# Performance work log

Hardware: AMD Instinct MI355X
Metric: run time of the kernel (lower is better)

Reference implementation:

```python
import jax, jax.numpy as jnp
import numpy as np

B = 512; H = 84; W = 84; K = 20; DEPTH = 24; EMB = 512
FCS = 7 * 7 * 64
FLOW_C = 0.01


def _init(key, shape, fan_in):
    return jax.random.normal(key, shape, jnp.float32) * (1.0 / np.sqrt(fan_in))


def setup_inputs() -> dict:
    key = jax.random.key(0)
    ks = jax.random.split(key, 22)
    return {
        "inp": jax.random.normal(ks[0], (B, 2, H, W), jnp.float32),
        "cw1": _init(ks[1], (32, 2, 8, 8), 2 * 8 * 8),
        "cb1": jnp.zeros((32,), jnp.float32),
        "cw2": _init(ks[2], (64, 32, 4, 4), 32 * 4 * 4),
        "cb2": jnp.zeros((64,), jnp.float32),
        "cw3": _init(ks[3], (64, 64, 3, 3), 64 * 3 * 3),
        "cb3": jnp.zeros((64,), jnp.float32),
        "fcw": _init(ks[4], (EMB, FCS), FCS),
        "fcb": jnp.zeros((EMB,), jnp.float32),
        "otw": _init(ks[5], (K * 2, EMB), EMB),
        "otb": jnp.zeros((K * 2,), jnp.float32),
        "ctw": _init(ks[6], (2, EMB), EMB),
        "ctb": jnp.zeros((2,), jnp.float32),
        "m1w": _init(ks[7], (21 * 21 * DEPTH, EMB), EMB),
        "m1b": jnp.zeros((21 * 21 * DEPTH,), jnp.float32),
        "c1w": _init(ks[8], (DEPTH, DEPTH, 3, 3), DEPTH * 9),
        "c1b": jnp.zeros((DEPTH,), jnp.float32),
        "c2w": _init(ks[9], (DEPTH, DEPTH, 3, 3), DEPTH * 9),
        "c2b": jnp.zeros((DEPTH,), jnp.float32),
        "c3w": _init(ks[10], (K, DEPTH, 1, 1), DEPTH),
        "c3b": jnp.zeros((K,), jnp.float32),
    }


def _conv(x, w, b, stride, pad):
    y = jax.lax.conv_general_dilated(
        x, w, (stride, stride), [(pad, pad), (pad, pad)],
        dimension_numbers=("NCHW", "OIHW", "NCHW"))
    return y + b[None, :, None, None]


def _up_mat(in_s, out_s):
    # bilinear, align_corners=True (torch UpsamplingBilinear2d)
    pos = jnp.arange(out_s, dtype=jnp.float32) * ((in_s - 1) / (out_s - 1))
    lo = jnp.clip(jnp.floor(pos).astype(jnp.int32), 0, in_s - 2)
    w = pos - lo.astype(jnp.float32)
    r = jnp.arange(out_s)
    M = jnp.zeros((out_s, in_s), jnp.float32)
    M = M.at[r, lo].add(1.0 - w).at[r, lo + 1].add(w)
    return M


def reference(inp, cw1, cb1, cw2, cb2, cw3, cb3, fcw, fcb, otw, otb,
              ctw, ctb, m1w, m1b, c1w, c1b, c2w, c2b, c3w, c3b):
    bs = inp.shape[0]
    # CNN encoder
    h1 = jax.nn.relu(_conv(inp, cw1, cb1, 4, 0))
    h2 = jax.nn.relu(_conv(h1, cw2, cb2, 2, 0))
    h3 = jax.nn.relu(_conv(h2, cw3, cb3, 1, 0))
    feat = h3.reshape(bs, -1)                              # [B, 3136]
    x = jax.nn.relu(feat @ fcw.T + fcb)                    # [B, EMB]
    # mask decoder
    m = (x @ m1w.T + m1b).reshape(bs, DEPTH, 21, 21)
    M42 = _up_mat(21, 42)
    m = jnp.einsum('bchw,Hh,Ww->bcHW', m, M42, M42)        # 21->42
    m = jax.nn.relu(m + _conv(m, c1w, c1b, 1, 1))
    M84 = _up_mat(42, 84)
    m = jnp.einsum('bchw,Hh,Ww->bcHW', m, M84, M84)        # 42->84
    m = jax.nn.relu(m + _conv(m, c2w, c2b, 1, 1))
    m = jax.nn.sigmoid(_conv(m, c3w, c3b, 1, 0))           # [B, K, 84, 84]
    # per-object translations -> flow
    ot = (x @ otw.T + otb).reshape(bs, K, 2)
    flow = jnp.einsum('bkhw,bkt->bthw', m, ot).reshape(bs, 2, H * W)
    ct = (x @ ctw.T + ctb)[:, :, None]                     # [B,2,1]
    flat_flow = flow + ct
    img_size_f = FLOW_C * jnp.array([[float(H)], [float(W)]], jnp.float32)
    # mesh grid: row 0 = y (row index), row 1 = x (col index)
    gy = jnp.repeat(jnp.arange(H, dtype=jnp.float32), W)
    gx = jnp.tile(jnp.arange(W, dtype=jnp.float32), H)
    grid = jnp.stack([gy, gx], 0)                          # [2, H*W]
    coords = img_size_f * flat_flow + grid
    ys = coords[:, 0, :].reshape(-1)                       # [B*H*W]
    xs = coords[:, 1, :].reshape(-1)
    # manual bilinear gather from second input frame
    src = inp[:, 1, :, :].reshape(-1)                      # [B*H*W] flat image
    x0 = jnp.clip(jnp.floor(xs).astype(jnp.int32), 0, W - 1)
    x1 = jnp.clip(x0 + 1, 0, W - 1)
    y0 = jnp.clip(jnp.floor(ys).astype(jnp.int32), 0, H - 1)
    y1 = jnp.clip(y0 + 1, 0, H - 1)
    base = jnp.repeat(jnp.arange(bs, dtype=jnp.int32) * (H * W), H * W)
    Ia = src[base + y0 * W + x0]
    Ib = src[base + y1 * W + x0]
    Ic = src[base + y0 * W + x1]
    Id = src[base + y1 * W + x1]
    xc = jnp.clip(xs, 0.0, float(W - 1))
    yc = jnp.clip(ys, 0.0, float(H - 1))
    x0f = x0.astype(jnp.float32); x1f = x1.astype(jnp.float32)
    y0f = y0.astype(jnp.float32); y1f = y1.astype(jnp.float32)
    out = ((x1f - xc) * (y1f - yc) * Ia + (x1f - xc) * (yc - y0f) * Ib +
           (xc - x0f) * (y1f - yc) * Ic + (xc - x0f) * (yc - y0f) * Id)
    return out.reshape(bs, 1, H, W)
```

## Files before the change

kernel.cpp:

```cpp
#include <hip/hip_runtime.h>
#include <math.h>

namespace {

typedef float f32x2 __attribute__((ext_vector_type(2)));
typedef float f32x4 __attribute__((ext_vector_type(4)));

#if defined(__has_builtin)
#if __has_builtin(__builtin_elementwise_fma)
#define HAVE_EW_FMA 1
#endif
#endif

__device__ __forceinline__ f32x2 pkfma(f32x2 a, f32x2 b, f32x2 c) {
#ifdef HAVE_EW_FMA
  return __builtin_elementwise_fma(a, b, c);
#else
  return a * b + c;
#endif
}
__device__ __forceinline__ f32x4 fma4(f32x4 a, f32x4 b, f32x4 c) {
#ifdef HAVE_EW_FMA
  return __builtin_elementwise_fma(a, b, c);
#else
  return a * b + c;
#endif
}

constexpr int IMS  = 84;
constexpr int NPIX = IMS * IMS;
constexpr int KOBJ = 20;

constexpr size_t OFF_X    = 0;
constexpr size_t OFF_OT   = 262144;
constexpr size_t OFF_CT   = 282624;
constexpr size_t OFF_WT2  = 283648;
constexpr size_t OFF_WT3  = 316416;
constexpr size_t OFF_M0   = 353280;
constexpr size_t OFF_R1   = 5772288;
constexpr size_t OFF_H1   = OFF_R1;
constexpr size_t OFF_H2   = 12325888;
constexpr size_t OFF_FEAT = 14980096;
constexpr size_t OFF_M1WT = OFF_H1;
constexpr size_t OFF_M1BT = OFF_H1 + 5419008;

__global__ void transpose_w(const float* __restrict__ w, float* __restrict__ wt,
                            int OC, int CKK) {
  int idx = blockIdx.x * 256 + threadIdx.x;
  if (idx < OC * CKK) {
    int oc = idx / CKK, ckk = idx % CKK;
    wt[ckk * OC + oc] = w[idx];
  }
}

__global__ __launch_bounds__(128) void permute_m1(
    const float* __restrict__ m1w, const float* __restrict__ m1b,
    float* __restrict__ wT, float* __restrict__ bT) {
  const int n = blockIdx.x;
  const int c = n / 441, rem = n % 441;
  const int np = rem * 24 + c;
  const float4* src = (const float4*)(m1w + (size_t)n * 512);
  float4* dst = (float4*)(wT + (size_t)np * 512);
  dst[threadIdx.x] = src[threadIdx.x];
  if (threadIdx.x == 0) bT[np] = m1b[n];
}

__global__ __launch_bounds__(256) void conv1_k(
    const float* __restrict__ inp, const float* __restrict__ w,
    const float* __restrict__ bias, float* __restrict__ out) {
  __shared__ __align__(16) float sIn[NPIX];
  __shared__ __align__(16) float sW[128 * 32];
  const int b = blockIdx.x, t = threadIdx.x;
  for (int i = t; i < 4096; i += 256) {
    int oc = i >> 7, ckk = i & 127;
    sW[ckk * 32 + oc] = w[i];
  }
  const float* ip = inp + (size_t)b * 2 * NPIX;
  const int oc0 = (t & 7) * 4;
  const int pg  = t >> 3;
  int ibase[13];
#pragma unroll
  for (int k = 0; k < 13; k++) {
    int p = pg + 32 * k; if (p > 399) p = 399;
    ibase[k] = (p / 20) * 4 * 84 + (p % 20) * 4;
  }
  f32x2 acc[13][2];
#pragma unroll
  for (int k = 0; k < 13; k++) { acc[k][0] = f32x2{0.f, 0.f}; acc[k][1] = f32x2{0.f, 0.f}; }
  for (int c = 0; c < 2; c++) {
    __syncthreads();
    for (int i = t; i < NPIX; i += 256) sIn[i] = ip[c * NPIX + i];
    __syncthreads();
    for (int u = 0; u < 8; u++) {
#pragma unroll
      for (int v = 0; v < 8; v++) {
        const float4 wv = *(const float4*)&sW[((c * 8 + u) * 8 + v) * 32 + oc0];
        const f32x2 w0 = {wv.x, wv.y}, w1 = {wv.z, wv.w};
        const int off = u * 84 + v;
#pragma unroll
        for (int k = 0; k < 13; k++) {
          float x = sIn[off + ibase[k]];
          f32x2 xv = {x, x};
          acc[k][0] = pkfma(w0, xv, acc[k][0]);
          acc[k][1] = pkfma(w1, xv, acc[k][1]);
        }
      }
    }
  }
  float b0 = bias[oc0], b1 = bias[oc0+1], b2 = bias[oc0+2], b3 = bias[oc0+3];
  float* op = out + (size_t)b * 32 * 400;
#pragma unroll
  for (int k = 0; k < 13; k++) {
    int p = pg + 32 * k;
    if (p < 400) {
      op[(oc0+0)*400 + p] = fmaxf(acc[k][0][0] + b0, 0.f);
      op[(oc0+1)*400 + p] = fmaxf(acc[k][0][1] + b1, 0.f);
      op[(oc0+2)*400 + p] = fmaxf(acc[k][1][0] + b2, 0.f);
      op[(oc0+3)*400 + p] = fmaxf(acc[k][1][1] + b3, 0.f);
    }
  }
}

__global__ __launch_bounds__(256) void conv2_k(
    const float* __restrict__ in, const float* __restrict__ wt,
    const float* __restrict__ bias, float* __restrict__ out) {
  __shared__ float sIn[32 * 400];
  const int b = blockIdx.x, t = threadIdx.x;
  const float* ip = in + (size_t)b * 12800;
  for (int i = t; i < 12800; i += 256) sIn[i] = ip[i];
  __syncthreads();
  const int oc0 = (t & 7) * 8;
  const int pg  = t >> 3;
  int base[3];
#pragma unroll
  for (int k = 0; k < 3; k++) {
    int p = pg + 32 * k; if (p > 80) p = 80;
    base[k] = (p / 9) * 40 + (p % 9) * 2;
  }
  f32x2 acc[3][4];
#pragma unroll
  for (int k = 0; k < 3; k++)
#pragma unroll
    for (int o = 0; o < 4; o++) acc[k][o] = f32x2{0.f, 0.f};
  for (int c = 0; c < 32; c++) {
#pragma unroll
    for (int u = 0; u < 4; u++)
#pragma unroll
      for (int v = 0; v < 4; v++) {
        const float* wp = wt + ((c * 4 + u) * 4 + v) * 64 + oc0;
        float4 wa = *(const float4*)wp;
        float4 wb = *(const float4*)(wp + 4);
        const f32x2 w0 = {wa.x, wa.y}, w1 = {wa.z, wa.w};
        const f32x2 w2 = {wb.x, wb.y}, w3 = {wb.z, wb.w};
        int off = c * 400 + u * 20 + v;
#pragma unroll
        for (int k = 0; k < 3; k++) {
          float x = sIn[off + base[k]];
          f32x2 xv = {x, x};
          acc[k][0] = pkfma(w0, xv, acc[k][0]);
          acc[k][1] = pkfma(w1, xv, acc[k][1]);
          acc[k][2] = pkfma(w2, xv, acc[k][2]);
          acc[k][3] = pkfma(w3, xv, acc[k][3]);
        }
      }
  }
  float* op = out + (size_t)b * 5184;
#pragma unroll
  for (int k = 0; k < 3; k++) {
    int p = pg + 32 * k;
    if (p < 81) {
#pragma unroll
      for (int o = 0; o < 8; o++)
        op[(oc0+o)*81 + p] = fmaxf(acc[k][o >> 1][o & 1] + bias[oc0+o], 0.f);
    }
  }
}

__global__ __launch_bounds__(256) void conv3_k(
    const float* __restrict__ in, const float* __restrict__ wt,
    const float* __restrict__ bias, float* __restrict__ out) {
  __shared__ float sIn[64 * 81];
  const int b = blockIdx.x, t = threadIdx.x;
  const float* ip = in + (size_t)b * 5184;
  for (int i = t; i < 5184; i += 256) sIn[i] = ip[i];
  __syncthreads();
  const int oc0 = (t & 7) * 8;
  const int pg  = t >> 3;
  int base[2];
#pragma unroll
  for (int k = 0; k < 2; k++) {
    int p = pg + 32 * k; if (p > 48) p = 48;
    base[k] = (p / 7) * 9 + (p % 7);
  }
  f32x2 acc[2][4];
#pragma unroll
  for (int k = 0; k < 2; k++)
#pragma unroll
    for (int o = 0; o < 4; o++) acc[k][o] = f32x2{0.f, 0.f};
  for (int c = 0; c < 64; c++) {
#pragma unroll
    for (int u = 0; u < 3; u++)
#pragma unroll
      for (int v = 0; v < 3; v++) {
        const float* wp = wt + ((c * 3 + u) * 3 + v) * 64 + oc0;
        float4 wa = *(const float4*)wp;
        float4 wb = *(const float4*)(wp + 4);
        const f32x2 w0 = {wa.x, wa.y}, w1 = {wa.z, wa.w};
        const f32x2 w2 = {wb.x, wb.y}, w3 = {wb.z, wb.w};
        int off = c * 81 + u * 9 + v;
#pragma unroll
        for (int k = 0; k < 2; k++) {
          float x = sIn[off + base[k]];
          f32x2 xv = {x, x};
          acc[k][0] = pkfma(w0, xv, acc[k][0]);
          acc[k][1] = pkfma(w1, xv, acc[k][1]);
          acc[k][2] = pkfma(w2, xv, acc[k][2]);
          acc[k][3] = pkfma(w3, xv, acc[k][3]);
        }
      }
  }
  float* op = out + (size_t)b * 3136;
#pragma unroll
  for (int k = 0; k < 2; k++) {
    int p = pg + 32 * k;
    if (p < 49) {
#pragma unroll
      for (int o = 0; o < 8; o++)
        op[(oc0+o)*49 + p] = fmaxf(acc[k][o >> 1][o & 1] + bias[oc0+o], 0.f);
    }
  }
}

template<bool RELU>
__global__ __launch_bounds__(256) void gemm_k(
    const float* __restrict__ A, const float* __restrict__ Wm,
    const float* __restrict__ bias, float* __restrict__ C,
    int N, int K) {
  __shared__ __align__(16) float As[16][68];
  __shared__ __align__(16) float Ws[16][68];
  const int t = threadIdx.x;
  const int m0 = blockIdx.y * 64, n0 = blockIdx.x * 64;
  const int r  = t >> 2;
  const int kq = (t & 3) * 4;
  const int r0 = (t >> 4) * 4, c0 = (t & 15) * 4;
  f32x2 acc[4][2];
#pragma unroll
  for (int i = 0; i < 4; i++) { acc[i][0] = f32x2{0.f, 0.f}; acc[i][1] = f32x2{0.f, 0.f}; }
  for (int k0 = 0; k0 < K; k0 += 16) {
    float4 a = *(const float4*)(A + (size_t)(m0 + r) * K + k0 + kq);
    int wrow = n0 + r;
    float4 wv = make_float4(0.f, 0.f, 0.f, 0.f);
    if (wrow < N) wv = *(const float4*)(Wm + (size_t)wrow * K + k0 + kq);
    __syncthreads();
    As[kq+0][r] = a.x; As[kq+1][r] = a.y; As[kq+2][r] = a.z; As[kq+3][r] = a.w;
    Ws[kq+0][r] = wv.x; Ws[kq+1][r] = wv.y; Ws[kq+2][r] = wv.z; Ws[kq+3][r] = wv.w;
    __syncthreads();
#pragma unroll
    for (int kk = 0; kk < 16; kk++) {
      float4 av = *(const float4*)&As[kk][r0];
      float4 bv = *(const float4*)&Ws[kk][c0];
      const f32x2 b0 = {bv.x, bv.y}, b1 = {bv.z, bv.w};
      float ar[4] = {av.x, av.y, av.z, av.w};
#pragma unroll
      for (int i = 0; i < 4; i++) {
        f32x2 ai = {ar[i], ar[i]};
        acc[i][0] = pkfma(b0, ai, acc[i][0]);
        acc[i][1] = pkfma(b1, ai, acc[i][1]);
      }
    }
  }
#pragma unroll
  for (int i = 0; i < 4; i++) {
    int row = m0 + r0 + i;
#pragma unroll
    for (int j = 0; j < 4; j++) {
      int col = n0 + c0 + j;
      if (col < N) {
        float v = acc[i][j >> 1][j & 1] + bias[col];
        C[(size_t)row * N + col] = RELU ? fmaxf(v, 0.f) : v;
      }
    }
  }
}

__global__ __launch_bounds__(256) void gemm_splitk_k(
    const float* __restrict__ A, const float* __restrict__ Wm,
    float* __restrict__ Cpart, int N, int K, int Kslice) {
  __shared__ __align__(16) float As[16][68];
  __shared__ __align__(16) float Ws[16][68];
  const int t = threadIdx.x;
  const int m0 = blockIdx.y * 64, n0 = blockIdx.x * 64;
  const int kbeg = blockIdx.z * Kslice;
  const int kend = kbeg + Kslice;
  const int r  = t >> 2;
  const int kq = (t & 3) * 4;
  const int r0 = (t >> 4) * 4, c0 = (t & 15) * 4;
  f32x2 acc[4][2];
#pragma unroll
  for (int i = 0; i < 4; i++) { acc[i][0] = f32x2{0.f, 0.f}; acc[i][1] = f32x2{0.f, 0.f}; }
  for (int k0 = kbeg; k0 < kend; k0 += 16) {
    float4 a = *(const float4*)(A + (size_t)(m0 + r) * K + k0 + kq);
    float4 wv = *(const float4*)(Wm + (size_t)(n0 + r) * K + k0 + kq);
    __syncthreads();
    As[kq+0][r] = a.x; As[kq+1][r] = a.y; As[kq+2][r] = a.z; As[kq+3][r] = a.w;
    Ws[kq+0][r] = wv.x; Ws[kq+1][r] = wv.y; Ws[kq+2][r] = wv.z; Ws[kq+3][r] = wv.w;
    __syncthreads();
#pragma unroll
    for (int kk = 0; kk < 16; kk++) {
      float4 av = *(const float4*)&As[kk][r0];
      float4 bv = *(const float4*)&Ws[kk][c0];
      const f32x2 b0 = {bv.x, bv.y}, b1 = {bv.z, bv.w};
      float ar[4] = {av.x, av.y, av.z, av.w};
#pragma unroll
      for (int i = 0; i < 4; i++) {
        f32x2 ai = {ar[i], ar[i]};
        acc[i][0] = pkfma(b0, ai, acc[i][0]);
        acc[i][1] = pkfma(b1, ai, acc[i][1]);
      }
    }
  }
  float* cp = Cpart + (size_t)blockIdx.z * 512 * 512;
#pragma unroll
  for (int i = 0; i < 4; i++) {
    int row = m0 + r0 + i;
#pragma unroll
    for (int j = 0; j < 4; j++)
      cp[(size_t)row * N + n0 + c0 + j] = acc[i][j >> 1][j & 1];
  }
}

__global__ __launch_bounds__(256) void splitk_reduce_k(
    const float* __restrict__ Cpart, const float* __restrict__ bias,
    float* __restrict__ X) {
  int i4 = blockIdx.x * 256 + threadIdx.x;
  if (i4 < 65536) {
    int col4 = (i4 & 127) * 4;
    float4 p0 = *(const float4*)&Cpart[(size_t)i4 * 4];
    float4 p1 = *(const float4*)&Cpart[262144 + (size_t)i4 * 4];
    float4 p2 = *(const float4*)&Cpart[524288 + (size_t)i4 * 4];
    float4 p3 = *(const float4*)&Cpart[786432 + (size_t)i4 * 4];
    float4 bb = *(const float4*)&bias[col4];
    float4 o;
    o.x = fmaxf(p0.x + p1.x + p2.x + p3.x + bb.x, 0.f);
    o.y = fmaxf(p0.y + p1.y + p2.y + p3.y + bb.y, 0.f);
    o.z = fmaxf(p0.z + p1.z + p2.z + p3.z + bb.z, 0.f);
    o.w = fmaxf(p0.w + p1.w + p2.w + p3.w + bb.w, 0.f);
    *(float4*)&X[(size_t)i4 * 4] = o;
  }
}

__global__ __launch_bounds__(256) void gemm128_k(
    const float* __restrict__ A, const float* __restrict__ Wm,
    const float* __restrict__ bias, float* __restrict__ C,
    int N, int K) {
  __shared__ __align__(16) float As[16][132];
  __shared__ __align__(16) float Ws[16][132];
  const int t = threadIdx.x;
  const int m0 = blockIdx.y * 128, n0 = blockIdx.x * 128;
  const int lr = t >> 1;
  const int kq = (t & 1) * 8;
  const int r0 = (t >> 4) * 8, c0 = (t & 15) * 8;
  f32x2 acc[8][4];
#pragma unroll
  for (int i = 0; i < 8; i++)
#pragma unroll
    for (int j = 0; j < 4; j++) acc[i][j] = f32x2{0.f, 0.f};
  for (int k0 = 0; k0 < K; k0 += 16) {
    const float* ap = A + (size_t)(m0 + lr) * K + k0 + kq;
    float4 a0 = *(const float4*)ap;
    float4 a1 = *(const float4*)(ap + 4);
    int wrow = n0 + lr;
    float4 w0 = make_float4(0.f,0.f,0.f,0.f), w1 = make_float4(0.f,0.f,0.f,0.f);
    if (wrow < N) {
      const float* wp = Wm + (size_t)wrow * K + k0 + kq;
      w0 = *(const float4*)wp;
      w1 = *(const float4*)(wp + 4);
    }
    __syncthreads();
    As[kq+0][lr] = a0.x; As[kq+1][lr] = a0.y; As[kq+2][lr] = a0.z; As[kq+3][lr] = a0.w;
    As[kq+4][lr] = a1.x; As[kq+5][lr] = a1.y; As[kq+6][lr] = a1.z; As[kq+7][lr] = a1.w;
    Ws[kq+0][lr] = w0.x; Ws[kq+1][lr] = w0.y; Ws[kq+2][lr] = w0.z; Ws[kq+3][lr] = w0.w;
    Ws[kq+4][lr] = w1.x; Ws[kq+5][lr] = w1.y; Ws[kq+6][lr] = w1.z; Ws[kq+7][lr] = w1.w;
    __syncthreads();
#pragma unroll
    for (int kk = 0; kk < 16; kk++) {
      float4 av0 = *(const float4*)&As[kk][r0];
      float4 av1 = *(const float4*)&As[kk][r0 + 4];
      float4 bv0 = *(const float4*)&Ws[kk][c0];
      float4 bv1 = *(const float4*)&Ws[kk][c0 + 4];
      float ar[8] = {av0.x, av0.y, av0.z, av0.w, av1.x, av1.y, av1.z, av1.w};
      f32x2 br[4] = {{bv0.x, bv0.y}, {bv0.z, bv0.w}, {bv1.x, bv1.y}, {bv1.z, bv1.w}};
#pragma unroll
      for (int i = 0; i < 8; i++) {
        f32x2 ai = {ar[i], ar[i]};
#pragma unroll
        for (int j = 0; j < 4; j++) acc[i][j] = pkfma(br[j], ai, acc[i][j]);
      }
    }
  }
#pragma unroll
  for (int i = 0; i < 8; i++) {
    int row = m0 + r0 + i;
#pragma unroll
    for (int j = 0; j < 8; j++) {
      int col = n0 + c0 + j;
      if (col < N)
        C[(size_t)row * N + col] = acc[i][j >> 1][j & 1] + bias[col];
    }
  }
}

__global__ __launch_bounds__(384, 6) void upconv1_k(
    const float* __restrict__ X, const float* __restrict__ wt,
    const float* __restrict__ bias, float* __restrict__ outT) {
  constexpr int S_IN = 21, S_OUT = 42, TR = 6, UH = 8, UW = 44, NTILE = 7;
  __shared__ __align__(16) float sU[24 * UH * UW];
  const int b = blockIdx.x / NTILE;
  const int y0 = (blockIdx.x % NTILE) * TR;
  const int t = threadIdx.x;
  const float* xb = X + (size_t)b * 24 * S_IN * S_IN;
  const float sc = (float)(S_IN - 1) / (float)(S_OUT - 1);
  for (int rr = t; rr < UH * UW; rr += 384) {
    const int ry = rr / UW, cx = rr % UW;
    const int y = y0 + ry - 1, x = cx - 1;
    float* sdst = &sU[rr];
    if (y >= 0 && y < S_OUT && x >= 0 && x < S_OUT) {
      float py = y * sc, px = x * sc;
      int ly = (int)py; if (ly > S_IN - 2) ly = S_IN - 2;
      int lx = (int)px; if (lx > S_IN - 2) lx = S_IN - 2;
      float wy = py - (float)ly, wx = px - (float)lx;
      const f32x4 wx4 = {wx, wx, wx, wx};
      const f32x4 wy4 = {wy, wy, wy, wy};
      const float* p00 = xb + ((size_t)ly * S_IN + lx) * 24;
#pragma unroll
      for (int g = 0; g < 6; g++) {
        f32x4 q00 = *(const f32x4*)(p00 + 4 * g);
        f32x4 q01 = *(const f32x4*)(p00 + 24 + 4 * g);
        f32x4 q10 = *(const f32x4*)(p00 + 24 * S_IN + 4 * g);
        f32x4 q11 = *(const f32x4*)(p00 + 24 * S_IN + 24 + 4 * g);
        f32x4 ht = fma4(wx4, q01 - q00, q00);
        f32x4 hb = fma4(wx4, q11 - q10, q10);
        f32x4 v  = fma4(wy4, hb - ht, ht);
        sdst[(4*g + 0) * UH * UW] = v[0];
        sdst[(4*g + 1) * UH * UW] = v[1];
        sdst[(4*g + 2) * UH * UW] = v[2];
        sdst[(4*g + 3) * UH * UW] = v[3];
      }
    } else {
#pragma unroll
      for (int c = 0; c < 24; c++) sdst[c * UH * UW] = 0.f;
    }
  }
  __syncthreads();
  if (t < 252) {
    const int ry = t / 42, lx = t % 42;
    f32x2 acc[12];
#pragma unroll
    for (int j = 0; j < 12; j++) acc[j] = f32x2{0.f, 0.f};
    for (int ic = 0; ic < 24; ic++) {
      const float* urow = &sU[(ic * UH + ry) * UW + lx];
      const float* wp = wt + ic * 216;
#pragma unroll
      for (int ky = 0; ky < 3; ky++) {
        float x0v = urow[ky * UW + 0];
        float x1v = urow[ky * UW + 1];
        float x2v = urow[ky * UW + 2];
        f32x2 X0 = {x0v, x0v}, X1 = {x1v, x1v}, X2 = {x2v, x2v};
        const f32x2* wk2 = (const f32x2*)(wp + ky * 72);
#pragma unroll
        for (int j = 0; j < 12; j++)
          acc[j] = pkfma(wk2[j], X0,
                   pkfma(wk2[12 + j], X1,
                   pkfma(wk2[24 + j], X2, acc[j])));
      }
    }
    const int yy = y0 + ry;
    float* orow = outT + ((size_t)b * 1764 + yy * 42 + lx) * 24;
#pragma unroll
    for (int g = 0; g < 6; g++) {
      f32x4 u = { sU[((4*g + 0) * UH + ry + 1) * UW + lx + 1],
                  sU[((4*g + 1) * UH + ry + 1) * UW + lx + 1],
                  sU[((4*g + 2) * UH + ry + 1) * UW + lx + 1],
                  sU[((4*g + 3) * UH + ry + 1) * UW + lx + 1] };
      f32x4 a = {acc[2*g][0], acc[2*g][1], acc[2*g+1][0], acc[2*g+1][1]};
      f32x4 bb = *(const f32x4*)&bias[4*g];
      f32x4 s = u + a + bb;
      s[0] = fmaxf(s[0], 0.f); s[1] = fmaxf(s[1], 0.f);
      s[2] = fmaxf(s[2], 0.f); s[3] = fmaxf(s[3], 0.f);
      *(f32x4*)(orow + 4*g) = s;
    }
  }
}

__global__ __launch_bounds__(384, 6) void upconv2_final_k(
    const float* __restrict__ R1T, const float* __restrict__ inp,
    const float* __restrict__ wt, const float* __restrict__ bias,
    const float* __restrict__ c3w, const float* __restrict__ c3b,
    const float* __restrict__ ot, const float* __restrict__ ct,
    float* __restrict__ out) {
  constexpr int S_IN = 42, S_OUT = 84, TR = 6, UH = 8, TW = 42, UW = 44;
  __shared__ __align__(16) float sU[24 * UH * UW];
  const int blk = blockIdx.x;
  const int b = blk / 28;
  const int rr0 = blk % 28;
  const int y0 = (rr0 >> 1) * TR;
  const int x0 = (rr0 & 1) * TW;
  const int t = threadIdx.x;
  const float* xb = R1T + (size_t)b * 1764 * 24;
  const float sc = (float)(S_IN - 1) / (float)(S_OUT - 1);
  for (int rr = t; rr < UH * UW; rr += 384) {
    const int ry = rr / UW, cx = rr % UW;
    const int y = y0 + ry - 1, x = x0 + cx - 1;
    float* sdst = &sU[rr];
    if (y >= 0 && y < S_OUT && x >= 0 && x < S_OUT) {
      float py = y * sc, px = x * sc;
      int ly = (int)py; if (ly > S_IN - 2) ly = S_IN - 2;
      int lx = (int)px; if (lx > S_IN - 2) lx = S_IN - 2;
      float wy = py - (float)ly, wx = px - (float)lx;
      const f32x4 wx4 = {wx, wx, wx, wx};
      const f32x4 wy4 = {wy, wy, wy, wy};
      const float* p00 = xb + ((size_t)ly * S_IN + lx) * 24;
#pragma unroll
      for (int g = 0; g < 6; g++) {
        f32x4 q00 = *(const f32x4*)(p00 + 4 * g);
        f32x4 q01 = *(const f32x4*)(p00 + 24 + 4 * g);
        f32x4 q10 = *(const f32x4*)(p00 + 24 * S_IN + 4 * g);
        f32x4 q11 = *(const f32x4*)(p00 + 24 * S_IN + 24 + 4 * g);
        f32x4 ht = fma4(wx4, q01 - q00, q00);
        f32x4 hb = fma4(wx4, q11 - q10, q10);
        f32x4 v  = fma4(wy4, hb - ht, ht);
        sdst[(4*g + 0) * UH * UW] = v[0];
        sdst[(4*g + 1) * UH * UW] = v[1];
        sdst[(4*g + 2) * UH * UW] = v[2];
        sdst[(4*g + 3) * UH * UW] = v[3];
      }
    } else {
#pragma unroll
      for (int c = 0; c < 24; c++) sdst[c * UH * UW] = 0.f;
    }
  }
  __syncthreads();
  if (t < 252) {
    const int ry = t / 42, lx = t % 42;
    f32x2 acc[12];
#pragma unroll
    for (int j = 0; j < 12; j++) acc[j] = f32x2{0.f, 0.f};
    for (int ic = 0; ic < 24; ic++) {
      const float* urow = &sU[(ic * UH + ry) * UW + lx];
      const float* wp = wt + ic * 216;
#pragma unroll
      for (int ky = 0; ky < 3; ky++) {
        float x0v = urow[ky * UW + 0];
        float x1v = urow[ky * UW + 1];
        float x2v = urow[ky * UW + 2];
        f32x2 X0 = {x0v, x0v}, X1 = {x1v, x1v}, X2 = {x2v, x2v};
        const f32x2* wk2 = (const f32x2*)(wp + ky * 72);
#pragma unroll
        for (int j = 0; j < 12; j++)
          acc[j] = pkfma(wk2[j], X0,
                   pkfma(wk2[12 + j], X1,
                   pkfma(wk2[24 + j], X2, acc[j])));
      }
    }
    f32x2 r[12];
#pragma unroll
    for (int j = 0; j < 12; j++) {
      f32x2 u2 = { sU[((2*j)   * UH + ry + 1) * UW + lx + 1],
                   sU[((2*j+1) * UH + ry + 1) * UW + lx + 1] };
      f32x2 b2 = *(const f32x2*)&bias[2*j];
      f32x2 s = u2 + acc[j] + b2;
      r[j][0] = fmaxf(s[0], 0.f);
      r[j][1] = fmaxf(s[1], 0.f);
    }
    f32x2 f2 = *(const f32x2*)&ct[b * 2];
    const f32x2* ot2 = (const f32x2*)(ot + b * 2 * KOBJ);
    for (int k = 0; k < KOBJ; k++) {
      f32x2 zv = {c3b[k], 0.f};
      const f32x2* cw2 = (const f32x2*)(c3w + k * 24);
#pragma unroll
      for (int j = 0; j < 12; j++) zv = pkfma(r[j], cw2[j], zv);
      float z = zv[0] + zv[1];
      float m = 1.f / (1.f + __expf(-z));
      f32x2 mv = {m, m};
      f2 = pkfma(mv, ot2[k], f2);
    }
    const int gy = y0 + ry, gx = x0 + lx;
    const float imgf = 0.01f * 84.0f;
    float ys = imgf * f2[0] + (float)gy;
    float xs = imgf * f2[1] + (float)gx;
    int ix0 = (int)floorf(xs); ix0 = ix0 < 0 ? 0 : (ix0 > 83 ? 83 : ix0);
    int iy0 = (int)floorf(ys); iy0 = iy0 < 0 ? 0 : (iy0 > 83 ? 83 : iy0);
    int ix1 = ix0 + 1 > 83 ? 83 : ix0 + 1;
    int iy1 = iy0 + 1 > 83 ? 83 : iy0 + 1;
    float xc = fminf(fmaxf(xs, 0.f), 83.f);
    float yc = fminf(fmaxf(ys, 0.f), 83.f);
    float wx1 = (float)ix1 - xc, wx0 = xc - (float)ix0;
    float wy1 = (float)iy1 - yc, wy0 = yc - (float)iy0;
    const float* src = inp + ((size_t)b * 2 + 1) * NPIX;
    float Ia = src[iy0 * 84 + ix0], Ib = src[iy1 * 84 + ix0];
    float Ic = src[iy0 * 84 + ix1], Id = src[iy1 * 84 + ix1];
    out[(size_t)b * NPIX + gy * 84 + gx] =
        wx1 * wy1 * Ia + wx1 * wy0 * Ib + wx0 * wy1 * Ic + wx0 * wy0 * Id;
  }
}

}

extern "C" void kernel_launch(void* const* d_in, const int* in_sizes, int n_in,
                              void* d_out, int out_size, void* d_ws, size_t ws_size,
                              hipStream_t stream) {
  const float* inp = (const float*)d_in[0];
  const float* cw1 = (const float*)d_in[1];
  const float* cb1 = (const float*)d_in[2];
  const float* cw2 = (const float*)d_in[3];
  const float* cb2 = (const float*)d_in[4];
  const float* cw3 = (const float*)d_in[5];
  const float* cb3 = (const float*)d_in[6];
  const float* fcw = (const float*)d_in[7];
  const float* fcb = (const float*)d_in[8];
  const float* otw = (const float*)d_in[9];
  const float* otb = (const float*)d_in[10];
  const float* ctw = (const float*)d_in[11];
  const float* ctb = (const float*)d_in[12];
  const float* m1w = (const float*)d_in[13];
  const float* m1b = (const float*)d_in[14];
  const float* c1w = (const float*)d_in[15];
  const float* c1b = (const float*)d_in[16];
  const float* c2w = (const float*)d_in[17];
  const float* c2b = (const float*)d_in[18];
  const float* c3w = (const float*)d_in[19];
  const float* c3b = (const float*)d_in[20];
  float* W = (float*)d_ws;
  float* out = (float*)d_out;

  transpose_w<<<(64 * 512 + 255) / 256, 256, 0, stream>>>(cw2, W + OFF_WT2, 64, 512);
  transpose_w<<<(64 * 576 + 255) / 256, 256, 0, stream>>>(cw3, W + OFF_WT3, 64, 576);
  conv1_k<<<512, 256, 0, stream>>>(inp, cw1, cb1, W + OFF_H1);
  conv2_k<<<512, 256, 0, stream>>>(W + OFF_H1, W + OFF_WT2, cb2, W + OFF_H2);
  permute_m1<<<10584, 128, 0, stream>>>(m1w, m1b, W + OFF_M1WT, W + OFF_M1BT);
  conv3_k<<<512, 256, 0, stream>>>(W + OFF_H2, W + OFF_WT3, cb3, W + OFF_FEAT);
  transpose_w<<<(24 * 216 + 255) / 256, 256, 0, stream>>>(c1w, W + OFF_WT2, 24, 216);
  transpose_w<<<(24 * 216 + 255) / 256, 256, 0, stream>>>(c2w, W + OFF_WT3, 24, 216);
  gemm_splitk_k<<<dim3(8, 8, 4), 256, 0, stream>>>(W + OFF_FEAT, fcw, W + OFF_M0,
                                                   512, 3136, 784);
  splitk_reduce_k<<<256, 256, 0, stream>>>(W + OFF_M0, fcb, W + OFF_X);
  gemm_k<false><<<dim3(1, 8), 256, 0, stream>>>(W + OFF_X, otw, otb, W + OFF_OT, 40, 512);
  gemm_k<false><<<dim3(1, 8), 256, 0, stream>>>(W + OFF_X, ctw, ctb, W + OFF_CT, 2, 512);
  gemm128_k<<<dim3(83, 4), 256, 0, stream>>>(W + OFF_X, W + OFF_M1WT, W + OFF_M1BT,
                                             W + OFF_M0, 10584, 512);
  upconv1_k<<<512 * 7, 384, 0, stream>>>(W + OFF_M0, W + OFF_WT2, c1b, W + OFF_R1);
  upconv2_final_k<<<512 * 28, 384, 0, stream>>>(W + OFF_R1, inp, W + OFF_WT3, c2b,
                                                c3w, c3b, W + OFF_OT, W + OFF_CT, out);
}
```

Before: 1.076 ms.

## Split conv output channels across thread pairs, each computing two rows

Both upconv kernels change their thread-to-work mapping. Each thread now computes half of the 24 output channels (split by thread parity) for two vertically adjacent output rows instead of all channels for one row. Each loaded input value feeds both rows and each weight load is shared across two pixels, which cuts shared-memory and weight reads per FMA. In the final kernel the 1x1 conv reduction is completed with a lane shuffle between the pair, and only one thread of the pair does the warp sampling. This changes register pressure and the weight-load pattern, and the warp phase leaves half the threads idle.

```diff
diff --git a/kernel.cpp b/kernel.cpp
--- a/kernel.cpp
+++ b/kernel.cpp
@@ -453,41 +453,71 @@
   }
   __syncthreads();
   if (t < 252) {
-    const int ry = t / 42, lx = t % 42;
-    f32x2 acc[12];
-#pragma unroll
-    for (int j = 0; j < 12; j++) acc[j] = f32x2{0.f, 0.f};
+    const int h = t & 1;
+    const int u = t >> 1;
+    const int lx = u % 42, q = u / 42;
+    const int pr0 = 2 * q, pr1 = pr0 + 1;
+    f32x2 a0[6], a1[6];
+#pragma unroll
+    for (int j = 0; j < 6; j++) { a0[j] = f32x2{0.f, 0.f}; a1[j] = f32x2{0.f, 0.f}; }
+    const float* wph = wt + h * 12;
     for (int ic = 0; ic < 24; ic++) {
-      const float* urow = &sU[(ic * UH + ry) * UW + lx];
-      const float* wp = wt + ic * 216;
-#pragma unroll
-      for (int ky = 0; ky < 3; ky++) {
-        float x0v = urow[ky * UW + 0];
-        float x1v = urow[ky * UW + 1];
-        float x2v = urow[ky * UW + 2];
-        f32x2 X0 = {x0v, x0v}, X1 = {x1v, x1v}, X2 = {x2v, x2v};
-        const f32x2* wk2 = (const f32x2*)(wp + ky * 72);
-#pragma unroll
-        for (int j = 0; j < 12; j++)
-          acc[j] = pkfma(wk2[j], X0,
-                   pkfma(wk2[12 + j], X1,
-                   pkfma(wk2[24 + j], X2, acc[j])));
-      }
-    }
-    const int yy = y0 + ry;
-    float* orow = outT + ((size_t)b * 1764 + yy * 42 + lx) * 24;
-#pragma unroll
-    for (int g = 0; g < 6; g++) {
-      f32x4 u = { sU[((4*g + 0) * UH + ry + 1) * UW + lx + 1],
-                  sU[((4*g + 1) * UH + ry + 1) * UW + lx + 1],
-                  sU[((4*g + 2) * UH + ry + 1) * UW + lx + 1],
-                  sU[((4*g + 3) * UH + ry + 1) * UW + lx + 1] };
-      f32x4 a = {acc[2*g][0], acc[2*g][1], acc[2*g+1][0], acc[2*g+1][1]};
-      f32x4 bb = *(const f32x4*)&bias[4*g];
-      f32x4 s = u + a + bb;
-      s[0] = fmaxf(s[0], 0.f); s[1] = fmaxf(s[1], 0.f);
-      s[2] = fmaxf(s[2], 0.f); s[3] = fmaxf(s[3], 0.f);
-      *(f32x4*)(orow + 4*g) = s;
+      const float* ub = &sU[(ic * UH + pr0) * UW + lx];
+      float v[4][3];
+#pragma unroll
+      for (int r = 0; r < 4; r++)
+#pragma unroll
+        for (int kx = 0; kx < 3; kx++)
+          v[r][kx] = ub[r * UW + kx];
+      const float* wpc = wph + ic * 216;
+#pragma unroll
+      for (int ky = 0; ky < 3; ky++)
+#pragma unroll
+        for (int kx = 0; kx < 3; kx++) {
+          const float* wp = wpc + (ky * 3 + kx) * 24;
+          const f32x4 wA = *(const f32x4*)wp;
+          const f32x4 wB = *(const f32x4*)(wp + 4);
+          const f32x4 wC = *(const f32x4*)(wp + 8);
+          const f32x2 w0 = {wA[0], wA[1]}, w1 = {wA[2], wA[3]};
+          const f32x2 w2 = {wB[0], wB[1]}, w3 = {wB[2], wB[3]};
+          const f32x2 w4 = {wC[0], wC[1]}, w5 = {wC[2], wC[3]};
+          const f32x2 X0 = {v[ky][kx], v[ky][kx]};
+          const f32x2 X1 = {v[ky + 1][kx], v[ky + 1][kx]};
+          a0[0] = pkfma(w0, X0, a0[0]); a1[0] = pkfma(w0, X1, a1[0]);
+          a0[1] = pkfma(w1, X0, a0[1]); a1[1] = pkfma(w1, X1, a1[1]);
+          a0[2] = pkfma(w2, X0, a0[2]); a1[2] = pkfma(w2, X1, a1[2]);
+          a0[3] = pkfma(w3, X0, a0[3]); a1[3] = pkfma(w3, X1, a1[3]);
+          a0[4] = pkfma(w4, X0, a0[4]); a1[4] = pkfma(w4, X1, a1[4]);
+          a0[5] = pkfma(w5, X0, a0[5]); a1[5] = pkfma(w5, X1, a1[5]);
+        }
+    }
+    const int cb = h * 12;
+    const f32x4 bb0 = *(const f32x4*)&bias[cb];
+    const f32x4 bb1 = *(const f32x4*)&bias[cb + 4];
+    const f32x4 bb2 = *(const f32x4*)&bias[cb + 8];
+#pragma unroll
+    for (int px = 0; px < 2; px++) {
+      const int pr = px ? pr1 : pr0;
+      const f32x2* aa = px ? a1 : a0;
+      float o[12];
+#pragma unroll
+      for (int j = 0; j < 6; j++) {
+        float c0v = sU[((cb + 2*j)     * UH + pr + 1) * UW + lx + 1];
+        float c1v = sU[((cb + 2*j + 1) * UH + pr + 1) * UW + lx + 1];
+        o[2*j]   = c0v + aa[j][0];
+        o[2*j+1] = c1v + aa[j][1];
+      }
+      float* orow = outT + ((size_t)b * 1764 + (y0 + pr) * 42 + lx) * 24 + cb;
+      f32x4 s0 = {o[0], o[1], o[2], o[3]};   s0 += bb0;
+      f32x4 s1 = {o[4], o[5], o[6], o[7]};   s1 += bb1;
+      f32x4 s2 = {o[8], o[9], o[10], o[11]}; s2 += bb2;
+#pragma unroll
+      for (int e = 0; e < 4; e++) {
+        s0[e] = fmaxf(s0[e], 0.f); s1[e] = fmaxf(s1[e], 0.f); s2[e] = fmaxf(s2[e], 0.f);
+      }
+      *(f32x4*)(orow)     = s0;
+      *(f32x4*)(orow + 4) = s1;
+      *(f32x4*)(orow + 8) = s2;
     }
   }
 }
@@ -541,66 +571,110 @@
   }
   __syncthreads();
   if (t < 252) {
-    const int ry = t / 42, lx = t % 42;
-    f32x2 acc[12];
-#pragma unroll
-    for (int j = 0; j < 12; j++) acc[j] = f32x2{0.f, 0.f};
+    const int h = t & 1;
+    const int u = t >> 1;
+    const int lx = u % 42, q = u / 42;
+    const int pr0 = 2 * q, pr1 = pr0 + 1;
+    f32x2 a0[6], a1[6];
+#pragma unroll
+    for (int j = 0; j < 6; j++) { a0[j] = f32x2{0.f, 0.f}; a1[j] = f32x2{0.f, 0.f}; }
+    const float* wph = wt + h * 12;
     for (int ic = 0; ic < 24; ic++) {
-      const float* urow = &sU[(ic * UH + ry) * UW + lx];
-      const float* wp = wt + ic * 216;
-#pragma unroll
-      for (int ky = 0; ky < 3; ky++) {
-        float x0v = urow[ky * UW + 0];
-        float x1v = urow[ky * UW + 1];
-        float x2v = urow[ky * UW + 2];
-        f32x2 X0 = {x0v, x0v}, X1 = {x1v, x1v}, X2 = {x2v, x2v};
-        const f32x2* wk2 = (const f32x2*)(wp + ky * 72);
-#pragma unroll
-        for (int j = 0; j < 12; j++)
-          acc[j] = pkfma(wk2[j], X0,
-                   pkfma(wk2[12 + j], X1,
-                   pkfma(wk2[24 + j], X2, acc[j])));
-      }
-    }
-    f32x2 r[12];
-#pragma unroll
-    for (int j = 0; j < 12; j++) {
-      f32x2 u2 = { sU[((2*j)   * UH + ry + 1) * UW + lx + 1],
-                   sU[((2*j+1) * UH + ry + 1) * UW + lx + 1] };
-      f32x2 b2 = *(const f32x2*)&bias[2*j];
-      f32x2 s = u2 + acc[j] + b2;
-      r[j][0] = fmaxf(s[0], 0.f);
-      r[j][1] = fmaxf(s[1], 0.f);
-    }
-    f32x2 f2 = *(const f32x2*)&ct[b * 2];
-    const f32x2* ot2 = (const f32x2*)(ot + b * 2 * KOBJ);
+      const float* ub = &sU[(ic * UH + pr0) * UW + lx];
+      float v[4][3];
+#pragma unroll
+      for (int r = 0; r < 4; r++)
+#pragma unroll
+        for (int kx = 0; kx < 3; kx++)
+          v[r][kx] = ub[r * UW + kx];
+      const float* wpc = wph + ic * 216;
+#pragma unroll
+      for (int ky = 0; ky < 3; ky++)
+#pragma unroll
+        for (int kx = 0; kx < 3; kx++) {
+          const float* wp = wpc + (ky * 3 + kx) * 24;
+          const f32x4 wA = *(const f32x4*)wp;
+          const f32x4 wB = *(const f32x4*)(wp + 4);
+          const f32x4 wC = *(const f32x4*)(wp + 8);
+          const f32x2 w0 = {wA[0], wA[1]}, w1 = {wA[2], wA[3]};
+          const f32x2 w2 = {wB[0], wB[1]}, w3 = {wB[2], wB[3]};
+          const f32x2 w4 = {wC[0], wC[1]}, w5 = {wC[2], wC[3]};
+          const f32x2 X0 = {v[ky][kx], v[ky][kx]};
+          const f32x2 X1 = {v[ky + 1][kx], v[ky + 1][kx]};
+          a0[0] = pkfma(w0, X0, a0[0]); a1[0] = pkfma(w0, X1, a1[0]);
+          a0[1] = pkfma(w1, X0, a0[1]); a1[1] = pkfma(w1, X1, a1[1]);
+          a0[2] = pkfma(w2, X0, a0[2]); a1[2] = pkfma(w2, X1, a1[2]);
+          a0[3] = pkfma(w3, X0, a0[3]); a1[3] = pkfma(w3, X1, a1[3]);
+          a0[4] = pkfma(w4, X0, a0[4]); a1[4] = pkfma(w4, X1, a1[4]);
+          a0[5] = pkfma(w5, X0, a0[5]); a1[5] = pkfma(w5, X1, a1[5]);
+        }
+    }
+    const int cb = h * 12;
+    f32x2 r0[6], r1[6];
+#pragma unroll
+    for (int j = 0; j < 6; j++) {
+      f32x2 b2 = *(const f32x2*)&bias[cb + 2*j];
+      f32x2 u0 = { sU[((cb + 2*j)     * UH + pr0 + 1) * UW + lx + 1],
+                   sU[((cb + 2*j + 1) * UH + pr0 + 1) * UW + lx + 1] };
+      f32x2 u1 = { sU[((cb + 2*j)     * UH + pr1 + 1) * UW + lx + 1],
+                   sU[((cb + 2*j + 1) * UH + pr1 + 1) * UW + lx + 1] };
+      f32x2 s0 = u0 + a0[j] + b2;
+      f32x2 s1 = u1 + a1[j] + b2;
+      r0[j][0] = fmaxf(s0[0], 0.f); r0[j][1] = fmaxf(s0[1], 0.f);
+      r1[j][0] = fmaxf(s1[0], 0.f); r1[j][1] = fmaxf(s1[1], 0.f);
+    }
+    float fy0 = ct[b * 2], fx0 = ct[b * 2 + 1];
+    float fy1 = fy0, fx1 = fx0;
+    const float* cwh = c3w + cb;
     for (int k = 0; k < KOBJ; k++) {
-      f32x2 zv = {c3b[k], 0.f};
-      const f32x2* cw2 = (const f32x2*)(c3w + k * 24);
-#pragma unroll
-      for (int j = 0; j < 12; j++) zv = pkfma(r[j], cw2[j], zv);
-      float z = zv[0] + zv[1];
-      float m = 1.f / (1.f + __expf(-z));
-      f32x2 mv = {m, m};
-      f2 = pkfma(mv, ot2[k], f2);
-    }
-    const int gy = y0 + ry, gx = x0 + lx;
-    const float imgf = 0.01f * 84.0f;
-    float ys = imgf * f2[0] + (float)gy;
-    float xs = imgf * f2[1] + (float)gx;
-    int ix0 = (int)floorf(xs); ix0 = ix0 < 0 ? 0 : (ix0 > 83 ? 83 : ix0);
-    int iy0 = (int)floorf(ys); iy0 = iy0 < 0 ? 0 : (iy0 > 83 ? 83 : iy0);
-    int ix1 = ix0 + 1 > 83 ? 83 : ix0 + 1;
-    int iy1 = iy0 + 1 > 83 ? 83 : iy0 + 1;
-    float xc = fminf(fmaxf(xs, 0.f), 83.f);
-    float yc = fminf(fmaxf(ys, 0.f), 83.f);
-    float wx1 = (float)ix1 - xc, wx0 = xc - (float)ix0;
-    float wy1 = (float)iy1 - yc, wy0 = yc - (float)iy0;
-    const float* src = inp + ((size_t)b * 2 + 1) * NPIX;
-    float Ia = src[iy0 * 84 + ix0], Ib = src[iy1 * 84 + ix0];
-    float Ic = src[iy0 * 84 + ix1], Id = src[iy1 * 84 + ix1];
-    out[(size_t)b * NPIX + gy * 84 + gx] =
-        wx1 * wy1 * Ia + wx1 * wy0 * Ib + wx0 * wy1 * Ic + wx0 * wy0 * Id;
+      const f32x4 cA = *(const f32x4*)(cwh + k * 24);
+      const f32x4 cB = *(const f32x4*)(cwh + k * 24 + 4);
+      const f32x4 cC = *(const f32x4*)(cwh + k * 24 + 8);
+      const f32x2 c0 = {cA[0], cA[1]}, c1 = {cA[2], cA[3]};
+      const f32x2 c2 = {cB[0], cB[1]}, c3 = {cB[2], cB[3]};
+      const f32x2 c4 = {cC[0], cC[1]}, c5 = {cC[2], cC[3]};
+      f32x2 z0v = r0[0] * c0; f32x2 z1v = r1[0] * c0;
+      z0v = pkfma(r0[1], c1, z0v); z1v = pkfma(r1[1], c1, z1v);
+      z0v = pkfma(r0[2], c2, z0v); z1v = pkfma(r1[2], c2, z1v);
+      z0v = pkfma(r0[3], c3, z0v); z1v = pkfma(r1[3], c3, z1v);
+      z0v = pkfma(r0[4], c4, z0v); z1v = pkfma(r1[4], c4, z1v);
+      z0v = pkfma(r0[5], c5, z0v); z1v = pkfma(r1[5], c5, z1v);
+      float z0 = z0v[0] + z0v[1];
+      float z1 = z1v[0] + z1v[1];
+      z0 += __shfl_xor(z0, 1);
+      z1 += __shfl_xor(z1, 1);
+      z0 += c3b[k]; z1 += c3b[k];
+      float m0 = 1.f / (1.f + __expf(-z0));
+      float m1 = 1.f / (1.f + __expf(-z1));
+      float oy = ot[b * 2 * KOBJ + 2 * k], ox = ot[b * 2 * KOBJ + 2 * k + 1];
+      fy0 += m0 * oy; fx0 += m0 * ox;
+      fy1 += m1 * oy; fx1 += m1 * ox;
+    }
+    if (h == 0) {
+      const float imgf = 0.01f * 84.0f;
+      const float* src = inp + ((size_t)b * 2 + 1) * NPIX;
+#pragma unroll
+      for (int px = 0; px < 2; px++) {
+        const int pr = px ? pr1 : pr0;
+        const float fy = px ? fy1 : fy0;
+        const float fx = px ? fx1 : fx0;
+        const int gy = y0 + pr, gx = x0 + lx;
+        float ys = imgf * fy + (float)gy;
+        float xs = imgf * fx + (float)gx;
+        int ix0 = (int)floorf(xs); ix0 = ix0 < 0 ? 0 : (ix0 > 83 ? 83 : ix0);
+        int iy0 = (int)floorf(ys); iy0 = iy0 < 0 ? 0 : (iy0 > 83 ? 83 : iy0);
+        int ix1 = ix0 + 1 > 83 ? 83 : ix0 + 1;
+        int iy1 = iy0 + 1 > 83 ? 83 : iy0 + 1;
+        float xc = fminf(fmaxf(xs, 0.f), 83.f);
+        float yc = fminf(fmaxf(ys, 0.f), 83.f);
+        float wx1 = (float)ix1 - xc, wx0 = xc - (float)ix0;
+        float wy1 = (float)iy1 - yc, wy0 = yc - (float)iy0;
+        float Ia = src[iy0 * 84 + ix0], Ib = src[iy1 * 84 + ix0];
+        float Ic = src[iy0 * 84 + ix1], Id = src[iy1 * 84 + ix1];
+        out[(size_t)b * NPIX + gy * 84 + gx] =
+            wx1 * wy1 * Ia + wx1 * wy0 * Ib + wx0 * wy1 * Ic + wx0 * wy0 * Id;
+      }
+    }
   }
 }
 
```

Measured after the change: 2.026 ms. 88.2% more time.
